# Kernel tuning notes

Measured on AMD Instinct MI355X. Metric: run time of the kernel, lower is better.

Reference implementation:

```python
import jax, jax.numpy as jnp
import numpy as np

DT_MIN, DT_MAX = 1e-3, 0.1
EPS = 1e-5

def rmsnorm(x, w):
    return x * jax.lax.rsqrt(jnp.mean(x * x, axis=-1, keepdims=True) + EPS) * w

def setup_inputs() -> dict:
    key = jax.random.key(0)
    ks = jax.random.split(key, 12)
    B, T, D = 1, 2048, 1024
    E, N, I, K = 2 * D, 64, 2048, 4
    s = lambda k, sh, fan: jax.random.normal(k, sh, jnp.float32) / np.sqrt(fan).astype(np.float32)
    return {
        'x': jax.random.normal(ks[0], (B, T, D), jnp.float32),
        'input_norm_w': jnp.ones((D,), jnp.float32),
        'ffn_norm_w': jnp.ones((D,), jnp.float32),
        'in_proj_W': s(ks[1], (D, 2 * E), D),
        'conv_W': s(ks[2], (K, 1, E), K),   # depthwise kernel, WIO layout
        'conv_b': jnp.zeros((E,), jnp.float32),
        'dt_W': s(ks[3], (E, E), E),
        'dt_b': jnp.zeros((E,), jnp.float32),
        'B_W': s(ks[4], (E, N), E),
        'C_W': s(ks[5], (E, N), E),
        'A_log': -jnp.log(jnp.arange(1, N + 1, dtype=jnp.float32)),
        'out_proj_W': s(ks[6], (E, D), E),
        'gate_W': s(ks[7], (D, I), D),
        'up_W': s(ks[8], (D, I), D),
        'down_W': s(ks[9], (I, D), I),
    }

def reference(x, input_norm_w, ffn_norm_w, in_proj_W, conv_W, conv_b, dt_W, dt_b,
              B_W, C_W, A_log, out_proj_W, gate_W, up_W, down_W):
    Bsz, T, D = x.shape
    E = in_proj_W.shape[1] // 2
    N = A_log.shape[0]
    # --- Mamba-2 branch (pre-norm) ---
    normed = rmsnorm(x, input_norm_w)
    xp = normed @ in_proj_W                      # [B,T,2E]
    x_z, z = xp[..., :E], xp[..., E:]
    # depthwise 1D conv over time, SAME padding
    xc = jax.lax.conv_general_dilated(
        x_z, conv_W, window_strides=(1,), padding='SAME',
        dimension_numbers=('NWC', 'WIO', 'NWC'), feature_group_count=E) + conv_b
    xc = jax.nn.silu(xc)                         # [B,T,E]
    dt = jnp.clip(jax.nn.softplus(xc @ dt_W + dt_b), DT_MIN, DT_MAX)  # [B,T,E]
    Bp = xc @ B_W                                # [B,T,N]
    Cp = xc @ C_W                                # [B,T,N]
    A = -jnp.exp(A_log)                          # [N]

    def step(h, ins):
        x_t, dt_t, B_t, C_t = ins                # [B,E],[B,E],[B,N],[B,N]
        dA = jnp.exp(dt_t[..., None] * A)        # [B,E,N]
        h = dA * h + (dt_t[..., None] * B_t[:, None, :]) * x_t[..., None]
        y_t = jnp.einsum('ben,bn->be', h, C_t)
        return h, y_t

    h0 = jnp.zeros((Bsz, E, N), x.dtype)
    _, y = jax.lax.scan(step, h0, (xc.transpose(1, 0, 2), dt.transpose(1, 0, 2),
                                   Bp.transpose(1, 0, 2), Cp.transpose(1, 0, 2)))
    y = y.transpose(1, 0, 2) * jax.nn.silu(z)    # [B,T,E]
    x = x + y @ out_proj_W                       # residual 1
    # --- SwiGLU FFN (pre-norm) ---
    n2 = rmsnorm(x, ffn_norm_w)
    ffn = (jax.nn.silu(n2 @ gate_W) * (n2 @ up_W)) @ down_W
    return x + ffn
```

## Files before the change

### kernel.cpp

```cpp
#include <hip/hip_runtime.h>
#include <hip/hip_bf16.h>

typedef __bf16 bf16x8 __attribute__((ext_vector_type(8)));
typedef __bf16 bf16x4 __attribute__((ext_vector_type(4)));
typedef float  f32x4  __attribute__((ext_vector_type(4)));

#define T_TOK 2048
#define DDIM  1024
#define EDIM  2048
#define NCHUNK 32
#define CKLEN  64

struct TJob { const float* src; __bf16* dst; int R, C, S, tilesX, tileOff; };
struct TJobs8 { TJob j[8]; };

__global__ __launch_bounds__(256)
void wprep_kernel(TJobs8 jobs)
{
    int tile = blockIdx.x;
    int ji = 0;
#pragma unroll
    for (int k = 1; k < 8; ++k) if (tile >= jobs.j[k].tileOff) ji = k;
    const TJob jb = jobs.j[ji];
    int rel = tile - jb.tileOff;
    int bx = rel % jb.tilesX, by = rel / jb.tilesX;
    __shared__ float tilebuf[32][33];
    const int tc0 = bx * 32, tr0 = by * 32;
    const int tx = threadIdx.x & 31, ty = threadIdx.x >> 5;
#pragma unroll
    for (int p = 0; p < 4; ++p) {
        int rl = ty + p * 8;
        tilebuf[rl][tx] = jb.src[(size_t)(tr0 + rl) * jb.S + tc0 + tx];
    }
    __syncthreads();
#pragma unroll
    for (int p = 0; p < 4; ++p) {
        int cl = ty + p * 8;
        float v = tilebuf[tx][cl];
        int c = tc0 + cl, r = tr0 + tx;
        jb.dst[(size_t)c * jb.R + r] = (__bf16)v;
    }
}

template<typename TS, typename TD>
__global__ __launch_bounds__(256)
void transpose_kernel(const TS* __restrict__ src, TD* __restrict__ dst,
                      int R, int C, int S, int dmul, int doff)
{
    __shared__ float tile[32][33];
    const int tc0 = blockIdx.x * 32, tr0 = blockIdx.y * 32;
    const int tx = threadIdx.x & 31, ty = threadIdx.x >> 5;
#pragma unroll
    for (int p = 0; p < 4; ++p) {
        int rl = ty + p * 8;
        tile[rl][tx] = (float)src[(size_t)(tr0 + rl) * S + tc0 + tx];
    }
    __syncthreads();
#pragma unroll
    for (int p = 0; p < 4; ++p) {
        int cl = ty + p * 8;
        float v = tile[tx][cl];
        int c = tc0 + cl, r = tr0 + tx;
        dst[((size_t)c * dmul + doff) * R + r] = (TD)v;
    }
}

__global__ __launch_bounds__(256)
void rmsnorm_kernel(const float* __restrict__ x, const float* __restrict__ w,
                    __bf16* __restrict__ out)
{
    const int row = blockIdx.x;
    const int t = threadIdx.x;
    float4 v = ((const float4*)(x + (size_t)row * DDIM))[t];
    float ss = v.x * v.x + v.y * v.y + v.z * v.z + v.w * v.w;
#pragma unroll
    for (int m = 32; m; m >>= 1) ss += __shfl_xor(ss, m);
    __shared__ float red[4];
    if ((t & 63) == 0) red[t >> 6] = ss;
    __syncthreads();
    float scale = rsqrtf((red[0] + red[1] + red[2] + red[3]) * (1.f / DDIM) + 1e-5f);
    float4 wv = ((const float4*)w)[t];
    __bf16* o = out + (size_t)row * DDIM + t * 4;
    o[0] = (__bf16)(v.x * scale * wv.x);
    o[1] = (__bf16)(v.y * scale * wv.y);
    o[2] = (__bf16)(v.z * scale * wv.z);
    o[3] = (__bf16)(v.w * scale * wv.w);
}

__global__ __launch_bounds__(256)
void conv_silu_kernel(const __bf16* __restrict__ xz, const float* __restrict__ W,
                      const float* __restrict__ b, __bf16* __restrict__ xc)
{
    int idx = blockIdx.x * 256 + threadIdx.x;
    int t = idx >> 11, e = idx & (EDIM - 1);
    float s = b[e];
#pragma unroll
    for (int k = 0; k < 4; ++k) {
        int tt = t - 1 + k;
        if (tt >= 0 && tt < T_TOK)
            s += (float)xz[(size_t)tt * EDIM + e] * W[k * EDIM + e];
    }
    s = s / (1.f + __expf(-s));
    xc[idx] = (__bf16)s;
}

__global__ __launch_bounds__(256)
void glu_kernel(const __bf16* __restrict__ gu, __bf16* __restrict__ outm)
{
    int idx = blockIdx.x * 256 + threadIdx.x;
    int t = idx >> 11, i = idx & 2047;
    float g = (float)gu[(size_t)t * 4096 + i];
    float u = (float)gu[(size_t)t * 4096 + 2048 + i];
    outm[idx] = (__bf16)(g / (1.f + __expf(-g)) * u);
}

template<int CTRL, int ROWMASK>
__device__ __forceinline__ float dpp_add(float v)
{
    int y = __builtin_amdgcn_update_dpp(0, __builtin_bit_cast(int, v),
                                        CTRL, ROWMASK, 0xf, true);
    return v + __builtin_bit_cast(float, y);
}


__global__ __launch_bounds__(512)
void scan1_kernel(const float* __restrict__ dtT, const __bf16* __restrict__ xcT,
                  const float* __restrict__ bc2, const float* __restrict__ A_log,
                  float* __restrict__ hend, float* __restrict__ dAp)
{
    __shared__ float  s_b[CKLEN * 64];
    __shared__ float  s_dt[16][CKLEN];
    __shared__ __bf16 s_x[16][CKLEN];
    const int tid = threadIdx.x;
    const int lane = tid & 63, w = tid >> 6;
    const int c = lane >> 5, i = lane & 31;
    const int ck = blockIdx.x & (NCHUNK - 1);
    const int eg = (blockIdx.x >> 5) * 16;

    {
#pragma unroll
        for (int r = 0; r < 2; ++r) {
            int linear = r * 512 + tid;
            int t = linear >> 4, k = linear & 15;
            *(float4*)&s_b[t * 64 + 4 * k] =
                *(const float4*)(bc2 + (size_t)(ck * CKLEN + t) * 128 + 4 * k);
        }
        if (tid < 256) {
            int ch = tid >> 4, k = tid & 15;
            *((float4*)&s_dt[ch][0] + k) =
                *(const float4*)(dtT + (size_t)(eg + ch) * T_TOK + ck * CKLEN + 4 * k);
        } else if (tid < 384) {
            int q = tid - 256, ch = q >> 3, k = q & 7;
            *((bf16x8*)&s_x[ch][0] + k) =
                *(const bf16x8*)(xcT + (size_t)(eg + ch) * T_TOK + ck * CKLEN + 8 * k);
        }
    }
    __syncthreads();

    const int ch = 2 * w + c;
    float2 al = *(const float2*)(A_log + 2 * i);
    const float L2E = 1.44269504f;
    const float An0 = -__expf(al.x) * L2E;
    const float An1 = -__expf(al.y) * L2E;
    float h0 = 0.f, h1 = 0.f, D = 0.f;

#pragma unroll 2
    for (int t0 = 0; t0 < CKLEN; t0 += 8) {
        float4 da = *(const float4*)&s_dt[ch][t0];
        float4 db = *(const float4*)&s_dt[ch][t0 + 4];
        bf16x8 x8 = *(const bf16x8*)&s_x[ch][t0];
        float dtv[8] = {da.x, da.y, da.z, da.w, db.x, db.y, db.z, db.w};
#pragma unroll
        for (int j = 0; j < 8; ++j) {
            float2 Bv = *(const float2*)&s_b[(t0 + j) * 64 + 2 * i];
            float u = dtv[j] * (float)x8[j];
            float dA0 = __builtin_amdgcn_exp2f(dtv[j] * An0);
            float dA1 = __builtin_amdgcn_exp2f(dtv[j] * An1);
            h0 = fmaf(dA0, h0, u * Bv.x);
            h1 = fmaf(dA1, h1, u * Bv.y);
            D += dtv[j];
        }
    }
    const int e = eg + ch;
    size_t idx = ((size_t)e * NCHUNK + ck) * 64 + 2 * i;
    *(float2*)(hend + idx) = make_float2(h0, h1);
    *(float2*)(dAp + idx)  = make_float2(__builtin_amdgcn_exp2f(An0 * D),
                                         __builtin_amdgcn_exp2f(An1 * D));
}

__global__ __launch_bounds__(256)
void scan_mid_kernel(float* __restrict__ hend_h0, const float* __restrict__ dAp)
{
    int gid = blockIdx.x * 256 + threadIdx.x;
    int e = gid >> 6, n = gid & 63;
    float h = 0.f;
#pragma unroll
    for (int ck = 0; ck < NCHUNK; ++ck) {
        size_t idx = ((size_t)e * NCHUNK + ck) * 64 + n;
        float he = hend_h0[idx];
        float P  = dAp[idx];
        hend_h0[idx] = h;
        h = P * h + he;
    }
}

__global__ __launch_bounds__(512)
void scan2_kernel(const float* __restrict__ dtT, const __bf16* __restrict__ xcT,
                  const __bf16* __restrict__ szT, const float* __restrict__ bc2,
                  const float* __restrict__ A_log, const float* __restrict__ h0s,
                  __bf16* __restrict__ y)
{
    __shared__ float  s_bp[CKLEN * 64];
    __shared__ float  s_cp[CKLEN * 64];
    __shared__ float  s_dt[32][68];
    __shared__ __bf16 s_x[32][72];
    __shared__ __bf16 s_y[CKLEN][36];
    const int tid = threadIdx.x;
    const int lane = tid & 63, w = tid >> 6;
    const int g = lane >> 4, i = lane & 15;
    const int ck = blockIdx.x & (NCHUNK - 1);
    const int eg = (blockIdx.x >> 5) * 32;

    {
#pragma unroll
        for (int r = 0; r < 2; ++r) {
            int linear = r * 512 + tid;
            int t = linear >> 4, k = linear & 15;
            const float* src = bc2 + (size_t)(ck * CKLEN + t) * 128 + 4 * k;
            *(float4*)&s_bp[t * 64 + 4 * k] = *(const float4*)src;
            *(float4*)&s_cp[t * 64 + 4 * k] = *(const float4*)(src + 64);
        }
        { int ch = tid >> 4, k = tid & 15;
          *(float4*)&s_dt[ch][4 * k] =
              *(const float4*)(dtT + (size_t)(eg + ch) * T_TOK + ck * CKLEN + 4 * k); }
        if (tid < 256) { int ch = tid >> 3, k = tid & 7;
          *(bf16x8*)&s_x[ch][8 * k] =
              *(const bf16x8*)(xcT + (size_t)(eg + ch) * T_TOK + ck * CKLEN + 8 * k); }
    }
    __syncthreads();

    const int ch = w * 4 + g;
    const int e = eg + ch;
    float4 al4 = *(const float4*)(A_log + 4 * i);
    const float L2E = 1.44269504f;
    const float An0 = -__expf(al4.x) * L2E;
    const float An1 = -__expf(al4.y) * L2E;
    const float An2 = -__expf(al4.z) * L2E;
    const float An3 = -__expf(al4.w) * L2E;
    float4 hh = *(const float4*)(h0s + ((size_t)e * NCHUNK + ck) * 64 + 4 * i);
    float h0 = hh.x, h1 = hh.y, h2 = hh.z, h3 = hh.w;

#pragma unroll 2
    for (int t0 = 0; t0 < CKLEN; t0 += 8) {
        float4 da = *(const float4*)&s_dt[ch][t0];
        float4 db = *(const float4*)&s_dt[ch][t0 + 4];
        bf16x8 x8 = *(const bf16x8*)&s_x[ch][t0];
        float dtv[8] = {da.x, da.y, da.z, da.w, db.x, db.y, db.z, db.w};
#pragma unroll
        for (int j = 0; j < 8; ++j) {
            float4 b0 = *(const float4*)&s_bp[(t0 + j) * 64 + 4 * i];
            float4 c0 = *(const float4*)&s_cp[(t0 + j) * 64 + 4 * i];
            float dt = dtv[j];
            float u = dt * (float)x8[j];
            h0 = fmaf(__builtin_amdgcn_exp2f(dt * An0), h0, u * b0.x);
            h1 = fmaf(__builtin_amdgcn_exp2f(dt * An1), h1, u * b0.y);
            h2 = fmaf(__builtin_amdgcn_exp2f(dt * An2), h2, u * b0.z);
            h3 = fmaf(__builtin_amdgcn_exp2f(dt * An3), h3, u * b0.w);
            float p = h0 * c0.x;
            p = fmaf(h1, c0.y, p);
            p = fmaf(h2, c0.z, p);
            p = fmaf(h3, c0.w, p);
            p = dpp_add<0x111, 0xf>(p);
            p = dpp_add<0x112, 0xf>(p);
            p = dpp_add<0x114, 0xf>(p);
            p = dpp_add<0x118, 0xf>(p);
            if (i == 15) s_y[t0 + j][ch] = (__bf16)p;
        }
    }
    __syncthreads();

    {
        int tt = tid >> 3, q = tid & 7;
        bf16x4 o;
#pragma unroll
        for (int d = 0; d < 4; ++d) {
            float zv = (float)szT[(size_t)(eg + 4 * q + d) * T_TOK + ck * CKLEN + tt];
            o[d] = (__bf16)((float)s_y[tt][4 * q + d] * zv);
        }
        *(bf16x4*)(y + (size_t)(ck * CKLEN + tt) * EDIM + eg + 4 * q) = o;
    }
}

__device__ __forceinline__ void glds16(const __bf16* g, __bf16* l)
{
    __builtin_amdgcn_global_load_lds(
        (const __attribute__((address_space(1))) unsigned*)g,
        (__attribute__((address_space(3))) unsigned*)l, 16, 0, 0);
}

template<int EPI>
__device__ __forceinline__ void gemm_epilogue(
    const f32x4& a, int row, int col, int N,
    void* Cout, void* Cout2, const float* res)
{
    if (EPI == 1) {
#pragma unroll
        for (int i = 0; i < 4; ++i)
            ((__bf16*)Cout)[(size_t)(row + i) * N + col] = (__bf16)a[i];
    } else if (EPI == 2) {
#pragma unroll
        for (int i = 0; i < 4; ++i) {
            size_t off = (size_t)(row + i) * N + col;
            ((float*)Cout)[off] = a[i] + res[off];
        }
    } else if (EPI == 3) {
        if (col < 2048) {
            float bias = res[col];
            float4 v;
            float* vv = (float*)&v;
#pragma unroll
            for (int i = 0; i < 4; ++i) {
                float s = a[i] + bias;
                s = (s > 20.f) ? s : log1pf(__expf(s));
                vv[i] = fminf(fmaxf(s, 0.001f), 0.1f);
            }
            *(float4*)((float*)Cout + (size_t)col * T_TOK + row) = v;
        } else {
#pragma unroll
            for (int i = 0; i < 4; ++i)
                ((float*)Cout2)[(size_t)(row + i) * 128 + (col - 2048)] = a[i];
        }
    } else if (EPI == 4) {
        if (col < 2048) {
#pragma unroll
            for (int i = 0; i < 4; ++i)
                ((__bf16*)Cout)[(size_t)(row + i) * EDIM + col] = (__bf16)a[i];
        } else {
            bf16x4 v;
#pragma unroll
            for (int i = 0; i < 4; ++i) {
                float s = a[i];
                v[i] = (__bf16)(s / (1.f + __expf(-s)));
            }
            *(bf16x4*)((__bf16*)Cout2 + (size_t)(col - 2048) * T_TOK + row) = v;
        }
    }
}

template<int EPI, int SWZ>
__global__ __launch_bounds__(256)
void gemm_kernel(const __bf16* __restrict__ A, const __bf16* __restrict__ Bt,
                 void* __restrict__ Cout, void* __restrict__ Cout2,
                 const float* __restrict__ res, int M, int N, int K)
{
    __shared__ __bf16 sAl[2 * 64 * 64];
    __shared__ __bf16 sBl[2 * 128 * 64];
    const int t = threadIdx.x;
    const int wave = t >> 6, lane = t & 63;
    int bx = blockIdx.x, by = blockIdx.y;
    if (SWZ) {
        int nwg = gridDim.x * gridDim.y;
        int bid = by * gridDim.x + bx;
        int cpx = nwg >> 3;
        int swz = (bid & 7) * cpx + (bid >> 3);
        bx = swz % gridDim.x;
        by = swz / gridDim.x;
    }
    const int brow = by * 64, bcol = bx * 128;
    const int wr = (wave >> 1) * 32, wc = (wave & 1) * 64;
    f32x4 acc[2][4] = {};

    const int rl8 = lane >> 3;
    const int ck8 = (lane & 7) ^ rl8;
    const __bf16* gA = A  + (size_t)(brow + wave * 16 + rl8) * K + ck8 * 8;
    const __bf16* gB = Bt + (size_t)(bcol + wave * 32 + rl8) * K + ck8 * 8;

    auto stage = [&](int buf, int k0) {
        __bf16* ba = sAl + buf * (64 * 64) + (wave * 16) * 64;
        __bf16* bb = sBl + buf * (128 * 64) + (wave * 32) * 64;
#pragma unroll
        for (int q = 0; q < 2; ++q)
            glds16(gA + (size_t)(q * 8) * K + k0, ba + q * 8 * 64);
#pragma unroll
        for (int q = 0; q < 4; ++q)
            glds16(gB + (size_t)(q * 8) * K + k0, bb + q * 8 * 64);
    };

    stage(0, 0);
    int cur = 0;
    for (int k0 = 0; k0 < K; k0 += 64) {
        __syncthreads();
        if (k0 + 64 < K) stage(cur ^ 1, k0 + 64);
        const __bf16* At = sAl + cur * (64 * 64);
        const __bf16* Btl = sBl + cur * (128 * 64);
#pragma unroll
        for (int ks = 0; ks < 2; ++ks) {
            const int rc = (((ks * 4 + (lane >> 4)) ^ (lane & 7))) * 8;
            bf16x8 af[2], bg[4];
#pragma unroll
            for (int m = 0; m < 2; ++m)
                af[m] = *(const bf16x8*)&At[(wr + m * 16 + (lane & 15)) * 64 + rc];
#pragma unroll
            for (int n = 0; n < 4; ++n)
                bg[n] = *(const bf16x8*)&Btl[(wc + n * 16 + (lane & 15)) * 64 + rc];
#pragma unroll
            for (int m = 0; m < 2; ++m)
#pragma unroll
                for (int n = 0; n < 4; ++n)
                    acc[m][n] = __builtin_amdgcn_mfma_f32_16x16x32_bf16(
                        af[m], bg[n], acc[m][n], 0, 0, 0);
        }
        cur ^= 1;
    }

    const int c_l = lane & 15, r_l = (lane >> 4) * 4;
#pragma unroll
    for (int m = 0; m < 2; ++m)
#pragma unroll
        for (int n = 0; n < 4; ++n)
            gemm_epilogue<EPI>(acc[m][n], brow + wr + m * 16 + r_l,
                               bcol + wc + n * 16 + c_l, N, Cout, Cout2, res);
}

template<int EPI>
__global__ __launch_bounds__(512)
void gemm_big(const __bf16* __restrict__ A, const __bf16* __restrict__ Bt,
              void* __restrict__ Cout, void* __restrict__ Cout2,
              const float* __restrict__ res, int M, int N, int K)
{
    __shared__ __bf16 sAl[2 * 256 * 64];
    __shared__ __bf16 sBl[2 * 128 * 64];
    const int t = threadIdx.x;
    const int w = t >> 6, lane = t & 63;
    const int brow = blockIdx.y * 256, bcol = blockIdx.x * 128;
    const int wr = (w >> 1) * 64, wc = (w & 1) * 64;
    f32x4 acc[4][4] = {};

    const int rl8 = lane >> 3;
    const int ck8 = (lane & 7) ^ rl8;
    const __bf16* gA = A  + (size_t)(brow + w * 32 + rl8) * K + ck8 * 8;
    const __bf16* gB = Bt + (size_t)(bcol + w * 16 + rl8) * K + ck8 * 8;

    auto stage = [&](int buf, int k0) {
        __bf16* ba = sAl + buf * (256 * 64) + (w * 32) * 64;
        __bf16* bb = sBl + buf * (128 * 64) + (w * 16) * 64;
#pragma unroll
        for (int q = 0; q < 4; ++q)
            glds16(gA + (size_t)(q * 8) * K + k0, ba + q * 8 * 64);
#pragma unroll
        for (int q = 0; q < 2; ++q)
            glds16(gB + (size_t)(q * 8) * K + k0, bb + q * 8 * 64);
    };

    stage(0, 0);
    int cur = 0;
    for (int k0 = 0; k0 < K; k0 += 64) {
        __syncthreads();
        if (k0 + 64 < K) stage(cur ^ 1, k0 + 64);
        const __bf16* At = sAl + cur * (256 * 64);
        const __bf16* Btl = sBl + cur * (128 * 64);
#pragma unroll
        for (int ks = 0; ks < 2; ++ks) {
            const int rchk = (((ks * 4 + (lane >> 4)) ^ (lane & 7))) * 8;
            bf16x8 af[4], bg[4];
#pragma unroll
            for (int m = 0; m < 4; ++m)
                af[m] = *(const bf16x8*)&At[(wr + m * 16 + (lane & 15)) * 64 + rchk];
#pragma unroll
            for (int n = 0; n < 4; ++n)
                bg[n] = *(const bf16x8*)&Btl[(wc + n * 16 + (lane & 15)) * 64 + rchk];
#pragma unroll
            for (int m = 0; m < 4; ++m)
#pragma unroll
                for (int n = 0; n < 4; ++n)
                    acc[m][n] = __builtin_amdgcn_mfma_f32_16x16x32_bf16(
                        af[m], bg[n], acc[m][n], 0, 0, 0);
        }
        cur ^= 1;
    }

    const int c_l = lane & 15, r_l = (lane >> 4) * 4;
#pragma unroll
    for (int m = 0; m < 4; ++m)
#pragma unroll
        for (int n = 0; n < 4; ++n)
            gemm_epilogue<EPI>(acc[m][n], brow + wr + m * 16 + r_l,
                               bcol + wc + n * 16 + c_l, N, Cout, Cout2, res);
}

extern "C" void kernel_launch(void* const* d_in, const int* in_sizes, int n_in,
                              void* d_out, int out_size, void* d_ws, size_t ws_size,
                              hipStream_t stream)
{
    (void)in_sizes; (void)n_in; (void)out_size; (void)ws_size;
    const float* x     = (const float*)d_in[0];
    const float* inw   = (const float*)d_in[1];
    const float* ffnw  = (const float*)d_in[2];
    const float* inpW  = (const float*)d_in[3];
    const float* convW = (const float*)d_in[4];
    const float* convB = (const float*)d_in[5];
    const float* dtW   = (const float*)d_in[6];
    const float* dtB   = (const float*)d_in[7];
    const float* BW    = (const float*)d_in[8];
    const float* CW    = (const float*)d_in[9];
    const float* Alog  = (const float*)d_in[10];
    const float* outpW = (const float*)d_in[11];
    const float* gateW = (const float*)d_in[12];
    const float* upW   = (const float*)d_in[13];
    const float* downW = (const float*)d_in[14];
    float* out = (float*)d_out;

    char* p = (char*)d_ws;
    auto alloc = [&](size_t n) { char* q = p; p += (n + 255) & ~(size_t)255; return q; };
    __bf16* wt_inproj = (__bf16*)alloc(4096ull * 1024 * 2);
    __bf16* wt_dtbc   = (__bf16*)alloc(2176ull * 2048 * 2);
    __bf16* wt_outp   = (__bf16*)alloc(1024ull * 2048 * 2);
    __bf16* wt_gu     = (__bf16*)alloc(4096ull * 1024 * 2);
    __bf16* wt_down   = (__bf16*)alloc(1024ull * 2048 * 2);
    __bf16* normed    = (__bf16*)alloc(2048ull * 1024 * 2);
    __bf16* xz        = (__bf16*)alloc(2048ull * 2048 * 2);
    __bf16* gu_buf    = (__bf16*)alloc(2048ull * 4096 * 2);
    __bf16* xc        = (__bf16*)alloc(2048ull * 2048 * 2);
    float*  scratch16 = (float*)alloc(2048ull * 2048 * 4);
    float*  bc        = (float*)alloc(2048ull * 128 * 4);
    float*  dtT       = (float*)alloc(2048ull * 2048 * 4);
    __bf16* xcT       = (__bf16*)alloc(2048ull * 2048 * 2);
    __bf16* szT       = (__bf16*)alloc(2048ull * 2048 * 2);
    float*  x2        = (float*)alloc(2048ull * 1024 * 4);

    dim3 B256(256);
    {
        TJobs8 tj;
        int off = 0, ji = 0;
        auto addjob = [&](const float* s, __bf16* d, int R, int C, int S) {
            tj.j[ji++] = TJob{s, d, R, C, S, C / 32, off};
            off += (C / 32) * (R / 32);
        };
        addjob(inpW,  wt_inproj, 1024, 4096, 4096);
        addjob(dtW,   wt_dtbc,   2048, 2048, 2048);
        addjob(BW,    wt_dtbc + 2048ull * 2048, 2048, 64, 64);
        addjob(CW,    wt_dtbc + 2112ull * 2048, 2048, 64, 64);
        addjob(outpW, wt_outp,   2048, 1024, 1024);
        addjob(gateW, wt_gu,     1024, 2048, 2048);
        addjob(upW,   wt_gu + 2048ull * 1024, 1024, 2048, 2048);
        addjob(downW, wt_down,   2048, 1024, 1024);
        wprep_kernel<<<dim3(off), B256, 0, stream>>>(tj);
    }

    rmsnorm_kernel<<<dim3(2048), B256, 0, stream>>>(x, inw, normed);
    gemm_big<4><<<dim3(32, 8), dim3(512), 0, stream>>>(normed, wt_inproj, xz, szT, nullptr, 2048, 4096, 1024);
    conv_silu_kernel<<<dim3(T_TOK * EDIM / 256), B256, 0, stream>>>(xz, convW, convB, xc);
    gemm_kernel<3, 1><<<dim3(17, 32), B256, 0, stream>>>(xc, wt_dtbc, dtT, bc, dtB, 2048, 2176, 2048);
    transpose_kernel<__bf16, __bf16><<<dim3(64, 64), B256, 0, stream>>>(xc, xcT, 2048, 2048, 2048, 1, 0);

    float* hend = scratch16;
    float* dAp  = (float*)gu_buf;
    scan1_kernel<<<dim3(4096), dim3(512), 0, stream>>>(dtT, xcT, bc, Alog, hend, dAp);
    scan_mid_kernel<<<dim3(512), B256, 0, stream>>>(hend, dAp);
    __bf16* y = xc;
    scan2_kernel<<<dim3(2048), dim3(512), 0, stream>>>(dtT, xcT, szT, bc, Alog, hend, y);

    gemm_kernel<2, 0><<<dim3(8, 32), B256, 0, stream>>>(y, wt_outp, x2, nullptr, x, 2048, 1024, 2048);
    rmsnorm_kernel<<<dim3(2048), B256, 0, stream>>>(x2, ffnw, normed);
    __bf16* gu = gu_buf;
    gemm_big<1><<<dim3(32, 8), dim3(512), 0, stream>>>(normed, wt_gu, gu, nullptr, nullptr, 2048, 4096, 1024);
    __bf16* ffnmid = (__bf16*)scratch16;
    glu_kernel<<<dim3(T_TOK * 2048 / 256), B256, 0, stream>>>(gu, ffnmid);
    gemm_kernel<2, 0><<<dim3(8, 32), B256, 0, stream>>>(ffnmid, wt_down, out, nullptr, x2, 2048, 1024, 2048);
}
```

Baseline: 323.9 us.

## Fuse SwiGLU into gate/up GEMM epilogue and transpose into conv-silu

New measurement: 304.0 us. -6.1%, faster.

```diff
diff --git a/kernel.cpp b/kernel.cpp
--- a/kernel.cpp
+++ b/kernel.cpp
@@ -11,7 +11,7 @@
 #define NCHUNK 32
 #define CKLEN  64
 
-struct TJob { const float* src; __bf16* dst; int R, C, S, tilesX, tileOff; };
+struct TJob { const float* src; __bf16* dst; int R, C, S, tilesX, tileOff, mode; };
 struct TJobs8 { TJob j[8]; };
 
 __global__ __launch_bounds__(256)
@@ -38,30 +38,9 @@
         int cl = ty + p * 8;
         float v = tilebuf[tx][cl];
         int c = tc0 + cl, r = tr0 + tx;
-        jb.dst[(size_t)c * jb.R + r] = (__bf16)v;
-    }
-}
-
-template<typename TS, typename TD>
-__global__ __launch_bounds__(256)
-void transpose_kernel(const TS* __restrict__ src, TD* __restrict__ dst,
-                      int R, int C, int S, int dmul, int doff)
-{
-    __shared__ float tile[32][33];
-    const int tc0 = blockIdx.x * 32, tr0 = blockIdx.y * 32;
-    const int tx = threadIdx.x & 31, ty = threadIdx.x >> 5;
-#pragma unroll
-    for (int p = 0; p < 4; ++p) {
-        int rl = ty + p * 8;
-        tile[rl][tx] = (float)src[(size_t)(tr0 + rl) * S + tc0 + tx];
-    }
-    __syncthreads();
-#pragma unroll
-    for (int p = 0; p < 4; ++p) {
-        int cl = ty + p * 8;
-        float v = tile[tx][cl];
-        int c = tc0 + cl, r = tr0 + tx;
-        dst[((size_t)c * dmul + doff) * R + r] = (TD)v;
+        int dr = (jb.mode == 0) ? c
+               : ((c >> 4) * 32 + (c & 15) + ((jb.mode == 2) ? 16 : 0));
+        jb.dst[(size_t)dr * jb.R + r] = (__bf16)v;
     }
 }
 
@@ -88,30 +67,51 @@
 }
 
 __global__ __launch_bounds__(256)
-void conv_silu_kernel(const __bf16* __restrict__ xz, const float* __restrict__ W,
-                      const float* __restrict__ b, __bf16* __restrict__ xc)
-{
-    int idx = blockIdx.x * 256 + threadIdx.x;
-    int t = idx >> 11, e = idx & (EDIM - 1);
-    float s = b[e];
+void conv_silu_xt_kernel(const __bf16* __restrict__ xz, const float* __restrict__ W,
+                         const float* __restrict__ b, __bf16* __restrict__ xc,
+                         __bf16* __restrict__ xcT)
+{
+    __shared__ __bf16 s_t[32][72];
+    const int tid = threadIdx.x;
+    const int e0 = blockIdx.x * 64, t0 = blockIdx.y * 32;
+    const int tl = tid >> 3, e8 = (tid & 7) * 8;
+    const int t = t0 + tl;
+    float acc[8];
+    {
+        float4 b0 = *(const float4*)(b + e0 + e8);
+        float4 b1 = *(const float4*)(b + e0 + e8 + 4);
+        acc[0] = b0.x; acc[1] = b0.y; acc[2] = b0.z; acc[3] = b0.w;
+        acc[4] = b1.x; acc[5] = b1.y; acc[6] = b1.z; acc[7] = b1.w;
+    }
 #pragma unroll
     for (int k = 0; k < 4; ++k) {
         int tt = t - 1 + k;
-        if (tt >= 0 && tt < T_TOK)
-            s += (float)xz[(size_t)tt * EDIM + e] * W[k * EDIM + e];
-    }
-    s = s / (1.f + __expf(-s));
-    xc[idx] = (__bf16)s;
-}
-
-__global__ __launch_bounds__(256)
-void glu_kernel(const __bf16* __restrict__ gu, __bf16* __restrict__ outm)
-{
-    int idx = blockIdx.x * 256 + threadIdx.x;
-    int t = idx >> 11, i = idx & 2047;
-    float g = (float)gu[(size_t)t * 4096 + i];
-    float u = (float)gu[(size_t)t * 4096 + 2048 + i];
-    outm[idx] = (__bf16)(g / (1.f + __expf(-g)) * u);
+        if (tt >= 0 && tt < T_TOK) {
+            bf16x8 v = *(const bf16x8*)(xz + (size_t)tt * EDIM + e0 + e8);
+            float4 w0 = *(const float4*)(W + k * EDIM + e0 + e8);
+            float4 w1 = *(const float4*)(W + k * EDIM + e0 + e8 + 4);
+            acc[0] += (float)v[0] * w0.x; acc[1] += (float)v[1] * w0.y;
+            acc[2] += (float)v[2] * w0.z; acc[3] += (float)v[3] * w0.w;
+            acc[4] += (float)v[4] * w1.x; acc[5] += (float)v[5] * w1.y;
+            acc[6] += (float)v[6] * w1.z; acc[7] += (float)v[7] * w1.w;
+        }
+    }
+    bf16x8 o;
+#pragma unroll
+    for (int j = 0; j < 8; ++j) {
+        float s = acc[j];
+        o[j] = (__bf16)(s / (1.f + __expf(-s)));
+    }
+    *(bf16x8*)(xc + (size_t)t * EDIM + e0 + e8) = o;
+    *(bf16x8*)&s_t[tl][e8] = o;
+    __syncthreads();
+    {
+        int el = tid >> 2, t8 = (tid & 3) * 8;
+        bf16x8 o2;
+#pragma unroll
+        for (int j = 0; j < 8; ++j) o2[j] = s_t[t8 + j][el];
+        *(bf16x8*)(xcT + (size_t)(e0 + el) * T_TOK + t0 + t8) = o2;
+    }
 }
 
 template<int CTRL, int ROWMASK>
@@ -480,12 +480,30 @@
     }
 
     const int c_l = lane & 15, r_l = (lane >> 4) * 4;
-#pragma unroll
-    for (int m = 0; m < 4; ++m)
-#pragma unroll
-        for (int n = 0; n < 4; ++n)
-            gemm_epilogue<EPI>(acc[m][n], brow + wr + m * 16 + r_l,
-                               bcol + wc + n * 16 + c_l, N, Cout, Cout2, res);
+    if constexpr (EPI == 5) {
+#pragma unroll
+        for (int m = 0; m < 4; ++m) {
+#pragma unroll
+            for (int n = 0; n < 4; n += 2) {
+                int row = brow + wr + m * 16 + r_l;
+                int fcol = (((bcol + wc + n * 16) >> 5) << 4) + c_l;
+#pragma unroll
+                for (int i = 0; i < 4; ++i) {
+                    float gg = acc[m][n][i];
+                    float uu = acc[m][n + 1][i];
+                    ((__bf16*)Cout)[(size_t)(row + i) * 2048 + fcol] =
+                        (__bf16)(gg / (1.f + __expf(-gg)) * uu);
+                }
+            }
+        }
+    } else {
+#pragma unroll
+        for (int m = 0; m < 4; ++m)
+#pragma unroll
+            for (int n = 0; n < 4; ++n)
+                gemm_epilogue<EPI>(acc[m][n], brow + wr + m * 16 + r_l,
+                                   bcol + wc + n * 16 + c_l, N, Cout, Cout2, res);
+    }
 }
 
 extern "C" void kernel_launch(void* const* d_in, const int* in_sizes, int n_in,
@@ -532,26 +550,25 @@
     {
         TJobs8 tj;
         int off = 0, ji = 0;
-        auto addjob = [&](const float* s, __bf16* d, int R, int C, int S) {
-            tj.j[ji++] = TJob{s, d, R, C, S, C / 32, off};
+        auto addjob = [&](const float* s, __bf16* d, int R, int C, int S, int mode) {
+            tj.j[ji++] = TJob{s, d, R, C, S, C / 32, off, mode};
             off += (C / 32) * (R / 32);
         };
-        addjob(inpW,  wt_inproj, 1024, 4096, 4096);
-        addjob(dtW,   wt_dtbc,   2048, 2048, 2048);
-        addjob(BW,    wt_dtbc + 2048ull * 2048, 2048, 64, 64);
-        addjob(CW,    wt_dtbc + 2112ull * 2048, 2048, 64, 64);
-        addjob(outpW, wt_outp,   2048, 1024, 1024);
-        addjob(gateW, wt_gu,     1024, 2048, 2048);
-        addjob(upW,   wt_gu + 2048ull * 1024, 1024, 2048, 2048);
-        addjob(downW, wt_down,   2048, 1024, 1024);
+        addjob(inpW,  wt_inproj, 1024, 4096, 4096, 0);
+        addjob(dtW,   wt_dtbc,   2048, 2048, 2048, 0);
+        addjob(BW,    wt_dtbc + 2048ull * 2048, 2048, 64, 64, 0);
+        addjob(CW,    wt_dtbc + 2112ull * 2048, 2048, 64, 64, 0);
+        addjob(outpW, wt_outp,   2048, 1024, 1024, 0);
+        addjob(gateW, wt_gu,     1024, 2048, 2048, 1);
+        addjob(upW,   wt_gu,     1024, 2048, 2048, 2);
+        addjob(downW, wt_down,   2048, 1024, 1024, 0);
         wprep_kernel<<<dim3(off), B256, 0, stream>>>(tj);
     }
 
     rmsnorm_kernel<<<dim3(2048), B256, 0, stream>>>(x, inw, normed);
     gemm_big<4><<<dim3(32, 8), dim3(512), 0, stream>>>(normed, wt_inproj, xz, szT, nullptr, 2048, 4096, 1024);
-    conv_silu_kernel<<<dim3(T_TOK * EDIM / 256), B256, 0, stream>>>(xz, convW, convB, xc);
+    conv_silu_xt_kernel<<<dim3(32, 64), B256, 0, stream>>>(xz, convW, convB, xc, xcT);
     gemm_kernel<3, 1><<<dim3(17, 32), B256, 0, stream>>>(xc, wt_dtbc, dtT, bc, dtB, 2048, 2176, 2048);
-    transpose_kernel<__bf16, __bf16><<<dim3(64, 64), B256, 0, stream>>>(xc, xcT, 2048, 2048, 2048, 1, 0);
 
     float* hend = scratch16;
     float* dAp  = (float*)gu_buf;
@@ -562,9 +579,7 @@
 
     gemm_kernel<2, 0><<<dim3(8, 32), B256, 0, stream>>>(y, wt_outp, x2, nullptr, x, 2048, 1024, 2048);
     rmsnorm_kernel<<<dim3(2048), B256, 0, stream>>>(x2, ffnw, normed);
-    __bf16* gu = gu_buf;
-    gemm_big<1><<<dim3(32, 8), dim3(512), 0, stream>>>(normed, wt_gu, gu, nullptr, nullptr, 2048, 4096, 1024);
     __bf16* ffnmid = (__bf16*)scratch16;
-    glu_kernel<<<dim3(T_TOK * 2048 / 256), B256, 0, stream>>>(gu, ffnmid);
+    gemm_big<5><<<dim3(32, 8), dim3(512), 0, stream>>>(normed, wt_gu, ffnmid, nullptr, nullptr, 2048, 4096, 1024);
     gemm_kernel<2, 0><<<dim3(8, 32), B256, 0, stream>>>(ffnmid, wt_down, out, nullptr, x2, 2048, 1024, 2048);
 }
```
